# Optimization experiments

Measured on AMD Instinct MI355X. Metric: run time of the kernel, lower is better.

Reference implementation:

```python
import jax, jax.numpy as jnp
import numpy as np

N = 50000   # nodes
E = 800000  # edges
D = 512     # channels (hidden_dim*2 == input_dim)
B = 64      # graphs in batch
L = 4       # GCN layers
OUT = 2
EPS = 1e-5


def setup_inputs() -> dict:
    key = jax.random.key(0)
    ks = jax.random.split(key, 12)
    x = jax.random.normal(ks[0], (N, D), jnp.float32)
    edge_index = jax.random.randint(ks[1], (2, E), 0, N, dtype=jnp.int64)
    batch = jnp.sort(jax.random.randint(ks[2], (N,), 0, B, dtype=jnp.int64))
    same_date = jax.random.randint(ks[3], (E,), 0, 2, dtype=jnp.int64)
    # parameters: 4 stacked GCNConv layers (same shape), BN stats, final linear
    Wc = jax.random.normal(ks[4], (L, D, D), jnp.float32) / np.float32(np.sqrt(D))
    bc = jax.random.normal(ks[5], (L, D), jnp.float32) * 0.01
    gamma = 1.0 + 0.1 * jax.random.normal(ks[6], (L, D), jnp.float32)
    beta = 0.1 * jax.random.normal(ks[7], (L, D), jnp.float32)
    rmean = 0.1 * jax.random.normal(ks[8], (L, D), jnp.float32)
    rvar = 0.5 + jax.random.uniform(ks[9], (L, D), jnp.float32)
    Wlin = jax.random.normal(ks[10], (2 * D, OUT), jnp.float32) / np.float32(np.sqrt(2 * D))
    blin = jnp.zeros((OUT,), jnp.float32)
    return {"x": x, "edge_index": edge_index, "batch": batch, "same_date": same_date,
            "Wc": Wc, "bc": bc, "gamma": gamma, "beta": beta, "rmean": rmean,
            "rvar": rvar, "Wlin": Wlin, "blin": blin}


def reference(x, edge_index, batch, same_date, Wc, bc, gamma, beta, rmean, rvar, Wlin, blin):
    # edge weights: 1.0 if same_date else 0.7
    w = jnp.where(same_date == 1, jnp.float32(1.0), jnp.float32(0.7))
    # GCN normalization with added self-loops (fill value 1.0)
    loops = jnp.arange(N, dtype=edge_index.dtype)
    row = jnp.concatenate([edge_index[0], loops])  # sources
    col = jnp.concatenate([edge_index[1], loops])  # targets
    ew = jnp.concatenate([w, jnp.ones((N,), jnp.float32)])
    deg = jax.ops.segment_sum(ew, col, num_segments=N)          # in-degree (weighted)
    dis = jax.lax.rsqrt(jnp.maximum(deg, EPS))                   # deg >= 1 from self-loops
    norm = dis[row] * ew * dis[col]                              # [E+N]

    h = x
    for i in range(L):
        hw = h @ Wc[i]                                           # [N, D]
        msg = hw[row] * norm[:, None]                            # gather + scale
        agg = jax.ops.segment_sum(msg, col, num_segments=N) + bc[i]
        # BatchNorm (inference: running stats) + ReLU; dropout is identity in eval
        h = gamma[i] * (agg - rmean[i]) * jax.lax.rsqrt(rvar[i] + EPS) + beta[i]
        h = jax.nn.relu(h)

    counts = jax.ops.segment_sum(jnp.ones((N,), jnp.float32), batch, num_segments=B)
    x_mean = jax.ops.segment_sum(h, batch, num_segments=B) / jnp.maximum(counts, 1.0)[:, None]
    x_max = jax.ops.segment_max(h, batch, num_segments=B)
    x_max = jnp.where(jnp.isfinite(x_max), x_max, 0.0)           # guard empty graphs
    z = jnp.concatenate([x_mean, x_max], axis=1) @ Wlin + blin   # [B, OUT]
    return jax.nn.log_softmax(z, axis=1)
```

## Files before the change

### kernel.cpp

```cpp
#include <hip/hip_runtime.h>
#include <hip/hip_bf16.h>

#define NN 50000
#define EE 800000
#define DD 512
#define BB 64
#define LL 4
#define OUTC 2
#define EPSV 1e-5f

#define MTG 64
#define NTG 512
#define BKG 32
#define HV8 (NN * DD / 8)

typedef _Float16 halfx8 __attribute__((ext_vector_type(8)));
typedef float floatx4 __attribute__((ext_vector_type(4)));
typedef float floatx2 __attribute__((ext_vector_type(2)));

#if defined(__has_builtin)
#if __has_builtin(__builtin_amdgcn_cvt_pk_f32_fp8) && __has_builtin(__builtin_amdgcn_cvt_pk_fp8_f32)
#define HW_FP8 1
#endif
#endif

#ifdef HW_FP8
__device__ __forceinline__ floatx2 f8x2_lo(unsigned int u) {
    return __builtin_amdgcn_cvt_pk_f32_fp8(u, 0);
}
__device__ __forceinline__ floatx2 f8x2_hi(unsigned int u) {
    return __builtin_amdgcn_cvt_pk_f32_fp8(u, 1);
}
__device__ __forceinline__ unsigned int f8_pack_lo(float a, float b, unsigned int old) {
    return (unsigned int)__builtin_amdgcn_cvt_pk_fp8_f32(a, b, (int)old, 0);
}
__device__ __forceinline__ unsigned int f8_pack_hi(float a, float b, unsigned int old) {
    return (unsigned int)__builtin_amdgcn_cvt_pk_fp8_f32(a, b, (int)old, 1);
}
__device__ __forceinline__ unsigned char f8_enc1(float v) {
    return (unsigned char)(__builtin_amdgcn_cvt_pk_fp8_f32(v, v, 0, 0) & 0xff);
}
#else
__device__ __forceinline__ float f8_dec1(unsigned int b) {
    unsigned int s = b & 0x80u, e = (b >> 3) & 15u, m = b & 7u;
    float v = e ? __uint_as_float(((e + 120u) << 23) | (m << 20))
                : (float)m * 0.001953125f;
    return s ? -v : v;
}
__device__ __forceinline__ floatx2 f8x2_lo(unsigned int u) {
    floatx2 r; r[0] = f8_dec1(u & 0xffu); r[1] = f8_dec1((u >> 8) & 0xffu); return r;
}
__device__ __forceinline__ floatx2 f8x2_hi(unsigned int u) {
    floatx2 r; r[0] = f8_dec1((u >> 16) & 0xffu); r[1] = f8_dec1((u >> 24) & 0xffu); return r;
}
__device__ __forceinline__ unsigned char f8_enc1(float x) {
    unsigned int s = (__float_as_uint(x) >> 24) & 0x80u;
    float a = fabsf(x);
    if (a < 0.015625f) {
        int m = (int)(a * 512.0f + 0.5f);
        return (unsigned char)(s | (unsigned int)m);
    }
    unsigned int ab = __float_as_uint(a);
    int e = (int)(ab >> 23) - 127;
    unsigned int m23 = ab & 0x7fffffu;
    unsigned int r = m23 + 0x7ffffu + ((m23 >> 20) & 1u);
    if (r >= 0x800000u) { e++; r -= 0x800000u; }
    unsigned int m = r >> 20;
    if (e > 8 || (e == 8 && m >= 7u)) return (unsigned char)(s | 0x7eu);
    return (unsigned char)(s | ((unsigned int)(e + 7) << 3) | m);
}
__device__ __forceinline__ unsigned int f8_pack_lo(float a, float b, unsigned int old) {
    return (old & 0xffff0000u) | (unsigned int)f8_enc1(a) | ((unsigned int)f8_enc1(b) << 8);
}
__device__ __forceinline__ unsigned int f8_pack_hi(float a, float b, unsigned int old) {
    return (old & 0x0000ffffu) | ((unsigned int)f8_enc1(a) << 16) | ((unsigned int)f8_enc1(b) << 24);
}
#endif

__device__ __forceinline__ floatx4 mfma16h(halfx8 a, halfx8 b, floatx4 c) {
    return __builtin_amdgcn_mfma_f32_16x16x32_f16(a, b, c, 0, 0, 0);
}

__device__ __forceinline__ void ldg2lds16(const _Float16* g, _Float16* l) {
    __builtin_amdgcn_global_load_lds(
        (const __attribute__((address_space(1))) unsigned int*)g,
        (__attribute__((address_space(3))) unsigned int*)l, 16, 0, 0);
}

__global__ void k_prep(const float* __restrict__ x, const float* __restrict__ Wc,
                       const int* __restrict__ ei, const int* __restrict__ sd,
                       const float* __restrict__ bc, const float* __restrict__ gamma,
                       const float* __restrict__ beta, const float* __restrict__ rmean,
                       const float* __restrict__ rvar,
                       unsigned char* __restrict__ X8, _Float16* __restrict__ WT,
                       float* __restrict__ deg, int* __restrict__ cnt,
                       float* __restrict__ scb, float* __restrict__ shb) {
    int i = blockIdx.x * blockDim.x + threadIdx.x;
    if (i < HV8) {
        const float4* xp = (const float4*)x + (size_t)i * 2;
        float4 v0 = xp[0], v1 = xp[1];
        unsigned int u0 = 0, u1 = 0;
        u0 = f8_pack_lo(v0.x, v0.y, u0);
        u0 = f8_pack_hi(v0.z, v0.w, u0);
        u1 = f8_pack_lo(v1.x, v1.y, u1);
        u1 = f8_pack_hi(v1.z, v1.w, u1);
        uint2 q; q.x = u0; q.y = u1;
        ((uint2*)X8)[i] = q;
    }
    if (i < LL * DD * DD) {
        int l = i >> 18;
        int rem = i & ((DD * DD) - 1);
        int k = rem >> 9;
        int n = rem & (DD - 1);
        WT[(l << 18) + (n << 9) + k] = (_Float16)Wc[i];
    }
    if (i < LL * DD) {
        float rs = rsqrtf(rvar[i] + EPSV);
        float scv = gamma[i] * rs;
        scb[i] = scv;
        shb[i] = scv * (bc[i] - rmean[i]) + beta[i];
    }
    if (i < EE) {
        int c = ei[EE + i];
        float w = (sd[i] == 1) ? 1.0f : 0.7f;
        atomicAdd(&deg[c], w);
        atomicAdd(&cnt[c], 1);
    }
}

__global__ void k_scan1(const int* __restrict__ cnt, int* __restrict__ rowptr,
                        int* __restrict__ bsum, const float* __restrict__ deg,
                        float* __restrict__ dis, const int* __restrict__ batch,
                        int* __restrict__ gstart, int* __restrict__ gend) {
    __shared__ int sh[256];
    const int t = threadIdx.x;
    const int i = blockIdx.x * 256 + t;
    if (i < NN) {
        dis[i] = rsqrtf(fmaxf(deg[i] + 1.0f, EPSV));
        int g = batch[i];
        int gp = (i == 0) ? -1 : batch[i - 1];
        if (g != gp) gstart[g] = i;
        int gn = (i == NN - 1) ? BB : batch[i + 1];
        if (g != gn) gend[g] = i + 1;
    }
    int v = (i < NN) ? cnt[i] : 0;
    sh[t] = v;
    __syncthreads();
    for (int off = 1; off < 256; off <<= 1) {
        int y = (t >= off) ? sh[t - off] : 0;
        __syncthreads();
        if (t >= off) sh[t] += y;
        __syncthreads();
    }
    if (i < NN) rowptr[i] = sh[t] - v;
    if (t == 255) bsum[blockIdx.x] = sh[255];
}

__global__ void k_scan2(int* __restrict__ bsum, int* __restrict__ rowptr, int nb) {
    __shared__ int sh[256];
    const int t = threadIdx.x;
    int v = (t < nb) ? bsum[t] : 0;
    sh[t] = v;
    __syncthreads();
    for (int off = 1; off < 256; off <<= 1) {
        int y = (t >= off) ? sh[t - off] : 0;
        __syncthreads();
        if (t >= off) sh[t] += y;
        __syncthreads();
    }
    if (t < nb) bsum[t] = sh[t] - v;
    if (t == 255) rowptr[NN] = sh[255];
}

__global__ void k_scan3(int* __restrict__ rowptr, const int* __restrict__ bsum) {
    int i = blockIdx.x * blockDim.x + threadIdx.x;
    if (i < NN) rowptr[i] += bsum[i >> 8];
}

__global__ void k_fill(const int* __restrict__ ei, const int* __restrict__ sd,
                       const float* __restrict__ dis, const int* __restrict__ rowptr,
                       int* __restrict__ fill, int* __restrict__ srcs,
                       float* __restrict__ enorm) {
    int e = blockIdx.x * blockDim.x + threadIdx.x;
    if (e >= EE) return;
    int s = ei[e];
    int c = ei[EE + e];
    float w = (sd[e] == 1) ? 1.0f : 0.7f;
    int p = rowptr[c] + atomicAdd(&fill[c], 1);
    srcs[p] = s;
    enorm[p] = dis[s] * w * dis[c];
}

__launch_bounds__(256)
__global__ void k_agg(const unsigned char* __restrict__ h8, const int* __restrict__ rowptr,
                      const int* __restrict__ srcs, const float* __restrict__ enorm,
                      const float* __restrict__ dis, _Float16* __restrict__ S) {
    const int n = blockIdx.x * 4 + (threadIdx.x >> 6);
    const int lane = threadIdx.x & 63;
    if (n >= NN) return;
    const float dn = dis[n];
    const float sw = dn * dn;
    uint2 q = ((const uint2*)(h8 + (size_t)n * DD))[lane];
    floatx2 acc[4];
    acc[0] = f8x2_lo(q.x) * sw;
    acc[1] = f8x2_hi(q.x) * sw;
    acc[2] = f8x2_lo(q.y) * sw;
    acc[3] = f8x2_hi(q.y) * sw;
    const int s0 = rowptr[n], s1 = rowptr[n + 1];
    int i = s0;
    for (; i + 8 <= s1; i += 8) {
        int sv[8];
        float wv[8];
        uint2 qv[8];
#pragma unroll
        for (int u = 0; u < 8; u++) { sv[u] = srcs[i + u]; wv[u] = enorm[i + u]; }
#pragma unroll
        for (int u = 0; u < 8; u++)
            qv[u] = ((const uint2*)(h8 + (size_t)sv[u] * DD))[lane];
#pragma unroll
        for (int u = 0; u < 8; u++) {
            acc[0] += f8x2_lo(qv[u].x) * wv[u];
            acc[1] += f8x2_hi(qv[u].x) * wv[u];
            acc[2] += f8x2_lo(qv[u].y) * wv[u];
            acc[3] += f8x2_hi(qv[u].y) * wv[u];
        }
    }
    for (; i + 4 <= s1; i += 4) {
        int sv[4];
        float wv[4];
        uint2 qv[4];
#pragma unroll
        for (int u = 0; u < 4; u++) { sv[u] = srcs[i + u]; wv[u] = enorm[i + u]; }
#pragma unroll
        for (int u = 0; u < 4; u++)
            qv[u] = ((const uint2*)(h8 + (size_t)sv[u] * DD))[lane];
#pragma unroll
        for (int u = 0; u < 4; u++) {
            acc[0] += f8x2_lo(qv[u].x) * wv[u];
            acc[1] += f8x2_hi(qv[u].x) * wv[u];
            acc[2] += f8x2_lo(qv[u].y) * wv[u];
            acc[3] += f8x2_hi(qv[u].y) * wv[u];
        }
    }
    for (; i < s1; i++) {
        uint2 qb = ((const uint2*)(h8 + (size_t)srcs[i] * DD))[lane];
        const float wn = enorm[i];
        acc[0] += f8x2_lo(qb.x) * wn;
        acc[1] += f8x2_hi(qb.x) * wn;
        acc[2] += f8x2_lo(qb.y) * wn;
        acc[3] += f8x2_hi(qb.y) * wn;
    }
    halfx8 hv;
#pragma unroll
    for (int k = 0; k < 4; k++) {
        hv[2 * k] = (_Float16)acc[k][0];
        hv[2 * k + 1] = (_Float16)acc[k][1];
    }
    ((halfx8*)(S + (size_t)n * DD))[lane] = hv;
}

template <int OUT8>
__launch_bounds__(512)
__global__ void k_gemm(const _Float16* __restrict__ A,
                       const _Float16* __restrict__ B,
                       const float* __restrict__ sc, const float* __restrict__ sh,
                       _Float16* __restrict__ C16, unsigned char* __restrict__ C8) {
    __shared__ _Float16 sA[MTG * BKG];
    __shared__ _Float16 sB[NTG * BKG];

    const int t = threadIdx.x;
    const int wid = t >> 6;
    const int lane = t & 63;
    const int l15 = lane & 15;
    const int quad = lane >> 4;
    const int m0 = blockIdx.x * MTG;
    const int wc = wid * 64;

    int arow = m0 + (t >> 2);
    if (arow > NN - 1) arow = NN - 1;
    const _Float16* gA = A + (size_t)arow * DD + (t & 3) * 8;
    _Float16* lA = sA + t * 8;
    const _Float16* gB = B + (size_t)(t >> 2) * DD + (t & 3) * 8;
    _Float16* lB = sB + t * 8;

    floatx4 acc[4][4];
#pragma unroll
    for (int i = 0; i < 4; i++)
#pragma unroll
        for (int j = 0; j < 4; j++) acc[i][j] = (floatx4){0.f, 0.f, 0.f, 0.f};

    for (int k0 = 0; k0 < DD; k0 += BKG) {
        __syncthreads();
        if (t < 256) ldg2lds16(gA + k0, lA);
#pragma unroll
        for (int r = 0; r < 4; r++)
            ldg2lds16(gB + (size_t)r * 128 * DD + k0, lB + r * 4096);
        __syncthreads();

        halfx8 a[4], b[4];
#pragma unroll
        for (int i = 0; i < 4; i++)
            a[i] = *(const halfx8*)&sA[(i * 16 + l15) * BKG + quad * 8];
#pragma unroll
        for (int j = 0; j < 4; j++)
            b[j] = *(const halfx8*)&sB[(wc + j * 16 + l15) * BKG + quad * 8];
#pragma unroll
        for (int i = 0; i < 4; i++)
#pragma unroll
            for (int j = 0; j < 4; j++)
                acc[i][j] = mfma16h(a[i], b[j], acc[i][j]);
    }

#pragma unroll
    for (int j = 0; j < 4; j++) {
        const int gcol = wc + j * 16 + l15;
        const float scv = sc[gcol];
        const float shv = sh[gcol];
#pragma unroll
        for (int i = 0; i < 4; i++) {
            const int rbase = m0 + i * 16 + quad * 4;
#pragma unroll
            for (int r = 0; r < 4; r++) {
                const int grow = rbase + r;
                if (grow < NN) {
                    float v = fmaxf(fmaf(scv, acc[i][j][r], shv), 0.f);
                    if (OUT8)
                        C8[(size_t)grow * DD + gcol] = f8_enc1(v);
                    else
                        C16[(size_t)grow * DD + gcol] = (_Float16)v;
                }
            }
        }
    }
}

__launch_bounds__(512)
__global__ void k_pool(const _Float16* __restrict__ H,
                       const int* __restrict__ gstart, const int* __restrict__ gend,
                       float* __restrict__ psum, unsigned int* __restrict__ pmax) {
    const int g = blockIdx.x;
    const int sl = blockIdx.y;
    const int c = threadIdx.x;
    const int s0 = gstart[g], e0 = gend[g];
    if (e0 <= s0) return;
    const int len = e0 - s0;
    const int chunk = (len + 7) >> 3;
    const int lo = s0 + sl * chunk;
    const int hi = min(lo + chunk, e0);
    float sum = 0.f, mx = 0.f;
    for (int n = lo; n < hi; n++) {
        float v = (float)H[(size_t)n * DD + c];
        sum += v;
        mx = fmaxf(mx, v);
    }
    if (lo < hi) {
        atomicAdd(&psum[g * DD + c], sum);
        atomicMax(&pmax[g * DD + c], __float_as_uint(fmaxf(mx, 0.f)));
    }
}

__launch_bounds__(64)
__global__ void k_final(const float* __restrict__ psum, const unsigned int* __restrict__ pmax,
                        const int* __restrict__ gstart, const int* __restrict__ gend,
                        const float* __restrict__ Wlin, const float* __restrict__ blin,
                        float* __restrict__ out) {
    const int g = blockIdx.x;
    const int lane = threadIdx.x;
    int cntg = gend[g] - gstart[g];
    if (cntg < 1) cntg = 1;
    const float inv = 1.0f / (float)cntg;
    float z0 = 0.f, z1 = 0.f;
#pragma unroll
    for (int j = 0; j < 8; j++) {
        const int k = j * 64 + lane;
        float mean = psum[g * DD + k] * inv;
        float mx = __uint_as_float(pmax[g * DD + k]);
        z0 += mean * Wlin[k * OUTC + 0] + mx * Wlin[(DD + k) * OUTC + 0];
        z1 += mean * Wlin[k * OUTC + 1] + mx * Wlin[(DD + k) * OUTC + 1];
    }
#pragma unroll
    for (int off = 32; off > 0; off >>= 1) {
        z0 += __shfl_down(z0, off);
        z1 += __shfl_down(z1, off);
    }
    if (lane == 0) {
        z0 += blin[0];
        z1 += blin[1];
        float m = fmaxf(z0, z1);
        float ls = m + logf(expf(z0 - m) + expf(z1 - m));
        out[g * OUTC + 0] = z0 - ls;
        out[g * OUTC + 1] = z1 - ls;
    }
}

extern "C" void kernel_launch(void* const* d_in, const int* in_sizes, int n_in,
                              void* d_out, int out_size, void* d_ws, size_t ws_size,
                              hipStream_t stream) {
    const float* x = (const float*)d_in[0];
    const int* ei = (const int*)d_in[1];
    const int* batch = (const int*)d_in[2];
    const int* sd = (const int*)d_in[3];
    const float* Wc = (const float*)d_in[4];
    const float* bc = (const float*)d_in[5];
    const float* gamma = (const float*)d_in[6];
    const float* beta = (const float*)d_in[7];
    const float* rmean = (const float*)d_in[8];
    const float* rvar = (const float*)d_in[9];
    const float* Wlin = (const float*)d_in[10];
    const float* blin = (const float*)d_in[11];
    float* out = (float*)d_out;

    char* p = (char*)d_ws;
    auto alloc = [&](size_t bytes) {
        char* r = p;
        p += (bytes + 255) & ~(size_t)255;
        return r;
    };
    unsigned char* X8 = (unsigned char*)alloc((size_t)NN * DD);
    _Float16* S = (_Float16*)alloc((size_t)NN * DD * 2);
    _Float16* WT = (_Float16*)alloc((size_t)LL * DD * DD * 2);
    float* scb = (float*)alloc(LL * DD * 4);
    float* shb = (float*)alloc(LL * DD * 4);
    char* zbase = p;
    float* deg = (float*)alloc(NN * 4);
    float* dis = (float*)alloc(NN * 4);
    int* cnt = (int*)alloc(NN * 4);
    int* fill = (int*)alloc(NN * 4);
    int* rowptr = (int*)alloc((NN + 1) * 4);
    int* bsum = (int*)alloc(256 * 4);
    int* srcs = (int*)alloc(EE * 4);
    float* enorm = (float*)alloc(EE * 4);
    int* gstart = (int*)alloc(BB * 4);
    int* gend = (int*)alloc(BB * 4);
    float* psum = (float*)alloc(BB * DD * 4);
    unsigned int* pmax = (unsigned int*)alloc(BB * DD * 4);
    size_t zbytes = (size_t)(p - zbase);
    (void)ws_size; (void)in_sizes; (void)n_in; (void)out_size;

    const int nb256 = (NN + 255) / 256;
    const int eb256 = (EE + 255) / 256;

    hipMemsetAsync(zbase, 0, zbytes, stream);
    k_prep<<<(HV8 + 255) / 256, 256, 0, stream>>>(x, Wc, ei, sd, bc, gamma, beta,
                                                  rmean, rvar, X8, WT, deg, cnt, scb, shb);
    k_scan1<<<nb256, 256, 0, stream>>>(cnt, rowptr, bsum, deg, dis, batch, gstart, gend);
    k_scan2<<<1, 256, 0, stream>>>(bsum, rowptr, nb256);
    k_scan3<<<nb256, 256, 0, stream>>>(rowptr, bsum);
    k_fill<<<eb256, 256, 0, stream>>>(ei, sd, dis, rowptr, fill, srcs, enorm);

    const int ggrid = (NN + MTG - 1) / MTG;
    for (int l = 0; l < LL; l++) {
        k_agg<<<(NN + 3) / 4, 256, 0, stream>>>(X8, rowptr, srcs, enorm, dis, S);
        if (l < LL - 1)
            k_gemm<1><<<ggrid, 512, 0, stream>>>(S, WT + (size_t)l * DD * DD,
                                                 scb + l * DD, shb + l * DD, nullptr, X8);
        else
            k_gemm<0><<<ggrid, 512, 0, stream>>>(S, WT + (size_t)l * DD * DD,
                                                 scb + l * DD, shb + l * DD, S, nullptr);
    }

    k_pool<<<dim3(BB, 8), 512, 0, stream>>>(S, gstart, gend, psum, pmax);
    k_final<<<BB, 64, 0, stream>>>(psum, pmax, gstart, gend, Wlin, blin, out);
}
```

Baseline: 810.8 us.

## Fuse neighbor aggregation into the GEMM kernel with an LDS-resident A tile

The separate aggregation kernel is merged into a per-layer kernel. Each block first gathers and aggregates 32 nodes into an fp16 A tile kept in shared memory, then runs the MFMA GEMM and the BN/ReLU epilogue on it. This removes the write and re-read of the full fp16 intermediate S each layer, using ping-pong fp8 buffers instead. Degree and count accumulation are packed into one 64-bit atomic with fixed-point weights, and the weight transpose now writes coalesced. The smaller M tile means the weight matrix is streamed twice as many times, and the gather latency is no longer overlapped by a separate kernel.

```diff
diff --git a/kernel.cpp b/kernel.cpp
--- a/kernel.cpp
+++ b/kernel.cpp
@@ -9,9 +9,8 @@
 #define OUTC 2
 #define EPSV 1e-5f
 
-#define MTG 64
-#define NTG 512
-#define BKG 32
+#define MT 32
+#define SA_CHH 1032
 #define HV8 (NN * DD / 8)
 
 typedef _Float16 halfx8 __attribute__((ext_vector_type(8)));
@@ -93,7 +92,7 @@
                        const float* __restrict__ beta, const float* __restrict__ rmean,
                        const float* __restrict__ rvar,
                        unsigned char* __restrict__ X8, _Float16* __restrict__ WT,
-                       float* __restrict__ deg, int* __restrict__ cnt,
+                       unsigned long long* __restrict__ degcnt,
                        float* __restrict__ scb, float* __restrict__ shb) {
     int i = blockIdx.x * blockDim.x + threadIdx.x;
     if (i < HV8) {
@@ -110,9 +109,9 @@
     if (i < LL * DD * DD) {
         int l = i >> 18;
         int rem = i & ((DD * DD) - 1);
-        int k = rem >> 9;
-        int n = rem & (DD - 1);
-        WT[(l << 18) + (n << 9) + k] = (_Float16)Wc[i];
+        int n = rem >> 9;
+        int k = rem & (DD - 1);
+        WT[i] = (_Float16)Wc[(l << 18) + (k << 9) + n];
     }
     if (i < LL * DD) {
         float rs = rsqrtf(rvar[i] + EPSV);
@@ -120,31 +119,37 @@
         scb[i] = scv;
         shb[i] = scv * (bc[i] - rmean[i]) + beta[i];
     }
-    if (i < EE) {
-        int c = ei[EE + i];
-        float w = (sd[i] == 1) ? 1.0f : 0.7f;
-        atomicAdd(&deg[c], w);
-        atomicAdd(&cnt[c], 1);
-    }
-}
-
-__global__ void k_scan1(const int* __restrict__ cnt, int* __restrict__ rowptr,
-                        int* __restrict__ bsum, const float* __restrict__ deg,
+    if ((i & 3) == 0) {
+        int e = i >> 2;
+        if (e < EE) {
+            int c = ei[EE + e];
+            unsigned long long v =
+                0x100000000ull + (unsigned long long)((sd[e] == 1) ? 10u : 7u);
+            atomicAdd(&degcnt[c], v);
+        }
+    }
+}
+
+__global__ void k_scan1(const unsigned long long* __restrict__ degcnt,
+                        int* __restrict__ rowptr, int* __restrict__ bsum,
                         float* __restrict__ dis, const int* __restrict__ batch,
                         int* __restrict__ gstart, int* __restrict__ gend) {
     __shared__ int sh[256];
     const int t = threadIdx.x;
     const int i = blockIdx.x * 256 + t;
+    int cntv = 0;
     if (i < NN) {
-        dis[i] = rsqrtf(fmaxf(deg[i] + 1.0f, EPSV));
+        unsigned long long dc = degcnt[i];
+        cntv = (int)(dc >> 32);
+        float degv = 0.1f * (float)(unsigned int)(dc & 0xffffffffu);
+        dis[i] = rsqrtf(fmaxf(degv + 1.0f, EPSV));
         int g = batch[i];
         int gp = (i == 0) ? -1 : batch[i - 1];
         if (g != gp) gstart[g] = i;
         int gn = (i == NN - 1) ? BB : batch[i + 1];
         if (g != gn) gend[g] = i + 1;
     }
-    int v = (i < NN) ? cnt[i] : 0;
-    sh[t] = v;
+    sh[t] = cntv;
     __syncthreads();
     for (int off = 1; off < 256; off <<= 1) {
         int y = (t >= off) ? sh[t - off] : 0;
@@ -152,7 +157,7 @@
         if (t >= off) sh[t] += y;
         __syncthreads();
     }
-    if (i < NN) rowptr[i] = sh[t] - v;
+    if (i < NN) rowptr[i] = sh[t] - cntv;
     if (t == 255) bsum[blockIdx.x] = sh[255];
 }
 
@@ -191,124 +196,124 @@
     enorm[p] = dis[s] * w * dis[c];
 }
 
-__launch_bounds__(256)
-__global__ void k_agg(const unsigned char* __restrict__ h8, const int* __restrict__ rowptr,
-                      const int* __restrict__ srcs, const float* __restrict__ enorm,
-                      const float* __restrict__ dis, _Float16* __restrict__ S) {
-    const int n = blockIdx.x * 4 + (threadIdx.x >> 6);
-    const int lane = threadIdx.x & 63;
-    if (n >= NN) return;
-    const float dn = dis[n];
-    const float sw = dn * dn;
-    uint2 q = ((const uint2*)(h8 + (size_t)n * DD))[lane];
-    floatx2 acc[4];
-    acc[0] = f8x2_lo(q.x) * sw;
-    acc[1] = f8x2_hi(q.x) * sw;
-    acc[2] = f8x2_lo(q.y) * sw;
-    acc[3] = f8x2_hi(q.y) * sw;
-    const int s0 = rowptr[n], s1 = rowptr[n + 1];
-    int i = s0;
-    for (; i + 8 <= s1; i += 8) {
-        int sv[8];
-        float wv[8];
-        uint2 qv[8];
-#pragma unroll
-        for (int u = 0; u < 8; u++) { sv[u] = srcs[i + u]; wv[u] = enorm[i + u]; }
-#pragma unroll
-        for (int u = 0; u < 8; u++)
-            qv[u] = ((const uint2*)(h8 + (size_t)sv[u] * DD))[lane];
-#pragma unroll
-        for (int u = 0; u < 8; u++) {
-            acc[0] += f8x2_lo(qv[u].x) * wv[u];
-            acc[1] += f8x2_hi(qv[u].x) * wv[u];
-            acc[2] += f8x2_lo(qv[u].y) * wv[u];
-            acc[3] += f8x2_hi(qv[u].y) * wv[u];
-        }
-    }
-    for (; i + 4 <= s1; i += 4) {
-        int sv[4];
-        float wv[4];
-        uint2 qv[4];
-#pragma unroll
-        for (int u = 0; u < 4; u++) { sv[u] = srcs[i + u]; wv[u] = enorm[i + u]; }
-#pragma unroll
-        for (int u = 0; u < 4; u++)
-            qv[u] = ((const uint2*)(h8 + (size_t)sv[u] * DD))[lane];
-#pragma unroll
-        for (int u = 0; u < 4; u++) {
-            acc[0] += f8x2_lo(qv[u].x) * wv[u];
-            acc[1] += f8x2_hi(qv[u].x) * wv[u];
-            acc[2] += f8x2_lo(qv[u].y) * wv[u];
-            acc[3] += f8x2_hi(qv[u].y) * wv[u];
-        }
-    }
-    for (; i < s1; i++) {
-        uint2 qb = ((const uint2*)(h8 + (size_t)srcs[i] * DD))[lane];
-        const float wn = enorm[i];
-        acc[0] += f8x2_lo(qb.x) * wn;
-        acc[1] += f8x2_hi(qb.x) * wn;
-        acc[2] += f8x2_lo(qb.y) * wn;
-        acc[3] += f8x2_hi(qb.y) * wn;
-    }
-    halfx8 hv;
-#pragma unroll
-    for (int k = 0; k < 4; k++) {
-        hv[2 * k] = (_Float16)acc[k][0];
-        hv[2 * k + 1] = (_Float16)acc[k][1];
-    }
-    ((halfx8*)(S + (size_t)n * DD))[lane] = hv;
-}
-
 template <int OUT8>
-__launch_bounds__(512)
-__global__ void k_gemm(const _Float16* __restrict__ A,
-                       const _Float16* __restrict__ B,
-                       const float* __restrict__ sc, const float* __restrict__ sh,
-                       _Float16* __restrict__ C16, unsigned char* __restrict__ C8) {
-    __shared__ _Float16 sA[MTG * BKG];
-    __shared__ _Float16 sB[NTG * BKG];
+__launch_bounds__(512, 4)
+__global__ void k_layer(const unsigned char* __restrict__ h8,
+                        const int* __restrict__ rowptr, const int* __restrict__ srcs,
+                        const float* __restrict__ enorm, const float* __restrict__ dis,
+                        const _Float16* __restrict__ B,
+                        const float* __restrict__ sc, const float* __restrict__ sh,
+                        _Float16* __restrict__ C16, unsigned char* __restrict__ C8) {
+    __shared__ _Float16 sA[16 * SA_CHH];
+    __shared__ _Float16 sB[512 * 32];
 
     const int t = threadIdx.x;
     const int wid = t >> 6;
     const int lane = t & 63;
     const int l15 = lane & 15;
     const int quad = lane >> 4;
-    const int m0 = blockIdx.x * MTG;
+    const int m0 = blockIdx.x * MT;
     const int wc = wid * 64;
 
-    int arow = m0 + (t >> 2);
-    if (arow > NN - 1) arow = NN - 1;
-    const _Float16* gA = A + (size_t)arow * DD + (t & 3) * 8;
-    _Float16* lA = sA + t * 8;
     const _Float16* gB = B + (size_t)(t >> 2) * DD + (t & 3) * 8;
     _Float16* lB = sB + t * 8;
 
-    floatx4 acc[4][4];
-#pragma unroll
-    for (int i = 0; i < 4; i++)
-#pragma unroll
-        for (int j = 0; j < 4; j++) acc[i][j] = (floatx4){0.f, 0.f, 0.f, 0.f};
-
-    for (int k0 = 0; k0 < DD; k0 += BKG) {
-        __syncthreads();
-        if (t < 256) ldg2lds16(gA + k0, lA);
-#pragma unroll
-        for (int r = 0; r < 4; r++)
-            ldg2lds16(gB + (size_t)r * 128 * DD + k0, lB + r * 4096);
-        __syncthreads();
-
-        halfx8 a[4], b[4];
-#pragma unroll
-        for (int i = 0; i < 4; i++)
-            a[i] = *(const halfx8*)&sA[(i * 16 + l15) * BKG + quad * 8];
+#pragma unroll
+    for (int r = 0; r < 4; r++)
+        ldg2lds16(gB + (size_t)r * 128 * DD, lB + r * 4096);
+
+    for (int s = 0; s < 4; s++) {
+        const int nl = wid * 4 + s;
+        int n = m0 + nl;
+        if (n > NN - 1) n = NN - 1;
+        const float dn = dis[n];
+        const float sw = dn * dn;
+        uint2 q = ((const uint2*)(h8 + (size_t)n * DD))[lane];
+        floatx2 acc[4];
+        acc[0] = f8x2_lo(q.x) * sw;
+        acc[1] = f8x2_hi(q.x) * sw;
+        acc[2] = f8x2_lo(q.y) * sw;
+        acc[3] = f8x2_hi(q.y) * sw;
+        const int s0 = rowptr[n], s1 = rowptr[n + 1];
+        int i = s0;
+        for (; i + 8 <= s1; i += 8) {
+            int sv[8];
+            float wv[8];
+            uint2 qv[8];
+#pragma unroll
+            for (int u = 0; u < 8; u++) { sv[u] = srcs[i + u]; wv[u] = enorm[i + u]; }
+#pragma unroll
+            for (int u = 0; u < 8; u++)
+                qv[u] = ((const uint2*)(h8 + (size_t)sv[u] * DD))[lane];
+#pragma unroll
+            for (int u = 0; u < 8; u++) {
+                acc[0] += f8x2_lo(qv[u].x) * wv[u];
+                acc[1] += f8x2_hi(qv[u].x) * wv[u];
+                acc[2] += f8x2_lo(qv[u].y) * wv[u];
+                acc[3] += f8x2_hi(qv[u].y) * wv[u];
+            }
+        }
+        for (; i + 4 <= s1; i += 4) {
+            int sv[4];
+            float wv[4];
+            uint2 qv[4];
+#pragma unroll
+            for (int u = 0; u < 4; u++) { sv[u] = srcs[i + u]; wv[u] = enorm[i + u]; }
+#pragma unroll
+            for (int u = 0; u < 4; u++)
+                qv[u] = ((const uint2*)(h8 + (size_t)sv[u] * DD))[lane];
+#pragma unroll
+            for (int u = 0; u < 4; u++) {
+                acc[0] += f8x2_lo(qv[u].x) * wv[u];
+                acc[1] += f8x2_hi(qv[u].x) * wv[u];
+                acc[2] += f8x2_lo(qv[u].y) * wv[u];
+                acc[3] += f8x2_hi(qv[u].y) * wv[u];
+            }
+        }
+        for (; i < s1; i++) {
+            uint2 qb = ((const uint2*)(h8 + (size_t)srcs[i] * DD))[lane];
+            const float wn = enorm[i];
+            acc[0] += f8x2_lo(qb.x) * wn;
+            acc[1] += f8x2_hi(qb.x) * wn;
+            acc[2] += f8x2_lo(qb.y) * wn;
+            acc[3] += f8x2_hi(qb.y) * wn;
+        }
+        halfx8 hv;
+#pragma unroll
+        for (int k = 0; k < 4; k++) {
+            hv[2 * k] = (_Float16)acc[k][0];
+            hv[2 * k + 1] = (_Float16)acc[k][1];
+        }
+        *(halfx8*)(sA + (lane >> 2) * SA_CHH + nl * 32 + (lane & 3) * 8) = hv;
+    }
+
+    floatx4 acc2[2][4];
+#pragma unroll
+    for (int i = 0; i < 2; i++)
+#pragma unroll
+        for (int j = 0; j < 4; j++) acc2[i][j] = (floatx4){0.f, 0.f, 0.f, 0.f};
+
+    for (int k0 = 0; k0 < DD; k0 += 32) {
+        __syncthreads();
+        const _Float16* sAc = sA + (k0 >> 5) * SA_CHH;
+        halfx8 a[2], b[4];
+#pragma unroll
+        for (int i = 0; i < 2; i++)
+            a[i] = *(const halfx8*)&sAc[(i * 16 + l15) * 32 + quad * 8];
 #pragma unroll
         for (int j = 0; j < 4; j++)
-            b[j] = *(const halfx8*)&sB[(wc + j * 16 + l15) * BKG + quad * 8];
-#pragma unroll
-        for (int i = 0; i < 4; i++)
+            b[j] = *(const halfx8*)&sB[(wc + j * 16 + l15) * 32 + quad * 8];
+        __syncthreads();
+        if (k0 + 32 < DD) {
+#pragma unroll
+            for (int r = 0; r < 4; r++)
+                ldg2lds16(gB + (size_t)r * 128 * DD + k0 + 32, lB + r * 4096);
+        }
+#pragma unroll
+        for (int i = 0; i < 2; i++)
 #pragma unroll
             for (int j = 0; j < 4; j++)
-                acc[i][j] = mfma16h(a[i], b[j], acc[i][j]);
+                acc2[i][j] = mfma16h(a[i], b[j], acc2[i][j]);
     }
 
 #pragma unroll
@@ -317,13 +322,13 @@
         const float scv = sc[gcol];
         const float shv = sh[gcol];
 #pragma unroll
-        for (int i = 0; i < 4; i++) {
+        for (int i = 0; i < 2; i++) {
             const int rbase = m0 + i * 16 + quad * 4;
 #pragma unroll
             for (int r = 0; r < 4; r++) {
                 const int grow = rbase + r;
                 if (grow < NN) {
-                    float v = fmaxf(fmaf(scv, acc[i][j][r], shv), 0.f);
+                    float v = fmaxf(fmaf(scv, acc2[i][j][r], shv), 0.f);
                     if (OUT8)
                         C8[(size_t)grow * DD + gcol] = f8_enc1(v);
                     else
@@ -416,15 +421,15 @@
         p += (bytes + 255) & ~(size_t)255;
         return r;
     };
-    unsigned char* X8 = (unsigned char*)alloc((size_t)NN * DD);
     _Float16* S = (_Float16*)alloc((size_t)NN * DD * 2);
+    unsigned char* X8a = (unsigned char*)S;
+    unsigned char* X8b = (unsigned char*)alloc((size_t)NN * DD);
     _Float16* WT = (_Float16*)alloc((size_t)LL * DD * DD * 2);
     float* scb = (float*)alloc(LL * DD * 4);
     float* shb = (float*)alloc(LL * DD * 4);
     char* zbase = p;
-    float* deg = (float*)alloc(NN * 4);
+    unsigned long long* degcnt = (unsigned long long*)alloc(NN * 8);
     float* dis = (float*)alloc(NN * 4);
-    int* cnt = (int*)alloc(NN * 4);
     int* fill = (int*)alloc(NN * 4);
     int* rowptr = (int*)alloc((NN + 1) * 4);
     int* bsum = (int*)alloc(256 * 4);
@@ -442,21 +447,27 @@
 
     hipMemsetAsync(zbase, 0, zbytes, stream);
     k_prep<<<(HV8 + 255) / 256, 256, 0, stream>>>(x, Wc, ei, sd, bc, gamma, beta,
-                                                  rmean, rvar, X8, WT, deg, cnt, scb, shb);
-    k_scan1<<<nb256, 256, 0, stream>>>(cnt, rowptr, bsum, deg, dis, batch, gstart, gend);
+                                                  rmean, rvar, X8a, WT, degcnt, scb, shb);
+    k_scan1<<<nb256, 256, 0, stream>>>(degcnt, rowptr, bsum, dis, batch, gstart, gend);
     k_scan2<<<1, 256, 0, stream>>>(bsum, rowptr, nb256);
     k_scan3<<<nb256, 256, 0, stream>>>(rowptr, bsum);
     k_fill<<<eb256, 256, 0, stream>>>(ei, sd, dis, rowptr, fill, srcs, enorm);
 
-    const int ggrid = (NN + MTG - 1) / MTG;
+    const int lgrid = (NN + MT - 1) / MT;
+    unsigned char* bufs[2] = {X8a, X8b};
+    int cur = 0;
     for (int l = 0; l < LL; l++) {
-        k_agg<<<(NN + 3) / 4, 256, 0, stream>>>(X8, rowptr, srcs, enorm, dis, S);
         if (l < LL - 1)
-            k_gemm<1><<<ggrid, 512, 0, stream>>>(S, WT + (size_t)l * DD * DD,
-                                                 scb + l * DD, shb + l * DD, nullptr, X8);
+            k_layer<1><<<lgrid, 512, 0, stream>>>(bufs[cur], rowptr, srcs, enorm, dis,
+                                                  WT + (size_t)l * DD * DD,
+                                                  scb + l * DD, shb + l * DD,
+                                                  nullptr, bufs[cur ^ 1]);
         else
-            k_gemm<0><<<ggrid, 512, 0, stream>>>(S, WT + (size_t)l * DD * DD,
-                                                 scb + l * DD, shb + l * DD, S, nullptr);
+            k_layer<0><<<lgrid, 512, 0, stream>>>(bufs[cur], rowptr, srcs, enorm, dis,
+                                                  WT + (size_t)l * DD * DD,
+                                                  scb + l * DD, shb + l * DD,
+                                                  S, nullptr);
+        cur ^= 1;
     }
 
     k_pool<<<dim3(BB, 8), 512, 0, stream>>>(S, gstart, gend, psum, pmax);
```

After: 860.6 us. 6.2% more time.
